# Kernel optimization log

Measured on AMD Instinct MI355X. Metric: run time of the kernel, lower is better.

The kernel has to match this reference:

```python
import jax, jax.numpy as jnp
import numpy as np

B, T, N, D, H, E = 64, 64, 32, 32, 128, 256


def setup_inputs() -> dict:
    key = jax.random.key(0)
    ks = jax.random.split(key, 20)

    def g(k, shape, scale=0.1):
        return (jax.random.normal(k, shape, dtype=jnp.float32) * scale)

    return {
        "ts_batch": jax.random.normal(ks[0], (B, T, N, D), dtype=jnp.float32),
        "edge_index": jax.random.randint(ks[1], (2, E), 0, N, dtype=jnp.int32),
        # encoder: 2-layer GCN-LSTM, gates packed as [i,f,g,o] -> 4H
        "Wen0": g(ks[2], (D + H, 4 * H)), "ben0": jnp.zeros((4 * H,), jnp.float32),
        "Wen1": g(ks[3], (2 * H, 4 * H)), "ben1": jnp.zeros((4 * H,), jnp.float32),
        # decoder: 2-layer GCN-LSTM
        "Wde0": g(ks[4], (D + H, 4 * H)), "bde0": jnp.zeros((4 * H,), jnp.float32),
        "Wde1": g(ks[5], (2 * H, 4 * H)), "bde1": jnp.zeros((4 * H,), jnp.float32),
        # per-node linears (the nn.ModuleList loops, batched as [N, in, out])
        "Wmu": g(ks[6], (N, H, H)), "bmu": jnp.zeros((N, H), jnp.float32),
        "Wlv": g(ks[7], (N, H, H)), "blv": jnp.zeros((N, H), jnp.float32),
        "Who": g(ks[8], (N, H, D)), "bho": jnp.zeros((N, D), jnp.float32),
        "Wholv": g(ks[9], (N, H, D)), "bholv": jnp.zeros((N, D), jnp.float32),
        # reparametrization noise (torch.randn_like), made explicit for determinism
        "eps": jax.random.normal(ks[10], (B, N, H), dtype=jnp.float32),
    }


def reference(ts_batch, edge_index, Wen0, ben0, Wen1, ben1, Wde0, bde0, Wde1, bde1,
              Wmu, bmu, Wlv, blv, Who, bho, Wholv, bholv, eps):
    n = Wmu.shape[0]
    # GCN normalized adjacency with self-loops: D^{-1/2}(A+I)D^{-1/2}
    A = jnp.zeros((n, n), jnp.float32).at[edge_index[1], edge_index[0]].add(1.0)
    A = A + jnp.eye(n, dtype=jnp.float32)
    dinv = jax.lax.rsqrt(A.sum(axis=1))
    A = dinv[:, None] * A * dinv[None, :]

    def gcn(x, W, b):  # x: [B,N,F] -> [B,N,4H]
        return jnp.einsum('ij,bjf->bif', A, x) @ W + b

    def cell(x, h, c, W, b):
        z = gcn(jnp.concatenate([x, h], axis=-1), W, b)
        i, f, g, o = jnp.split(z, 4, axis=-1)
        c = jax.nn.sigmoid(f) * c + jax.nn.sigmoid(i) * jnp.tanh(g)
        h = jax.nn.sigmoid(o) * jnp.tanh(c)
        return h, c

    def pnl(x, W, b):  # per-node linear, replaces the python loop over ModuleList
        return jnp.einsum('bnh,nho->bno', x, W) + b

    bsz, tlen = ts_batch.shape[0], ts_batch.shape[1]
    hdim = Wen0.shape[1] // 4
    z0 = jnp.zeros((bsz, n, hdim), jnp.float32)

    def enc_step(carry, x_t):
        h0, c0, h1, c1 = carry
        h0, c0 = cell(x_t, h0, c0, Wen0, ben0)
        h1, c1 = cell(h0, h1, c1, Wen1, ben1)
        return (h0, c0, h1, c1), None

    (h0, c0, h1, c1), _ = jax.lax.scan(
        enc_step, (z0, z0, z0, z0), jnp.transpose(ts_batch, (1, 0, 2, 3)))

    mu = pnl(h1, Wmu, bmu)
    logvar = pnl(h1, Wlv, blv)
    zlat = mu + eps * jnp.exp(logvar)  # reparametrize (note: exp(logvar), as in source)

    out_last = pnl(zlat, Who, bho)
    outlv_last = pnl(zlat, Wholv, bholv)

    # decoder initialized from encoder final (pre-reparam) hidden state; runs in
    # reverse time feeding back its own output (inference / no teacher forcing)
    def dec_step(carry, _):
        h0, c0, h1, c1, prev = carry
        h0, c0 = cell(prev, h0, c0, Wde0, bde0)
        h1, c1 = cell(h0, h1, c1, Wde1, bde1)
        out = pnl(h1, Who, bho)
        outlv = pnl(h1, Wholv, bholv)
        return (h0, c0, h1, c1, out), (out, outlv)

    _, (outs, outlvs) = jax.lax.scan(
        dec_step, (h0, c0, h1, c1, out_last), None, length=tlen - 1)

    # outs are for timesteps T-2 .. 0; reverse and append step T-1
    output = jnp.concatenate([outs[::-1], out_last[None]], axis=0)
    output_logvar = jnp.concatenate([outlvs[::-1], outlv_last[None]], axis=0)
    output = jnp.transpose(output, (1, 0, 2, 3))            # [B,T,N,D]
    output_logvar = jnp.transpose(output_logvar, (1, 0, 2, 3))
    return output, zlat, mu, logvar, output_logvar
```

## Files before the change

kernel.cpp:

```cpp
#include <hip/hip_runtime.h>


typedef unsigned short u16;
typedef unsigned int u32;
typedef short bf16x8 __attribute__((ext_vector_type(8)));
typedef float f32x4 __attribute__((ext_vector_type(4)));

#define O_OUT 0
#define O_Z   4194304
#define O_MU  4456448
#define O_LV  4718592
#define O_OLV 4980736

#define WS_ABF  0
#define WS_PEN0 1280
#define WS_PEN1 83200
#define WS_PDE0 214272
#define WS_PDE1 296192
#define WS_PHO  427264
#define WS_PLV  558336
#define WS_H1   689408
#define WS_NEED_BYTES 34408960ull

#define XSTR 552

__device__ __forceinline__ u16 f2b(float f){
  unsigned x = __float_as_uint(f);
  x += 0x7fffu + ((x>>16)&1u);
  return (u16)(x>>16);
}
__device__ __forceinline__ float b2f(u16 u){ return __uint_as_float(((unsigned)u)<<16); }
__device__ __forceinline__ float blo(unsigned u){ return __uint_as_float(u<<16); }
__device__ __forceinline__ float bhi(unsigned u){ return __uint_as_float(u & 0xffff0000u); }
__device__ __forceinline__ float sigm(float x){ return 1.f/(1.f+__expf(-x)); }
__device__ __forceinline__ float tanh_(float x){
  float e = __expf(-2.f*fabsf(x));
  float r = (1.f-e)/(1.f+e);
  return __builtin_copysignf(r, x);
}

__global__ void adj_kernel(const int* __restrict__ ei, u16* __restrict__ ws)
{
  __shared__ float As[1024];
  __shared__ float dinv[32];
  const int tid = threadIdx.x;
  for (int e = tid; e < 1024; e += 256) As[e] = 0.f;
  __syncthreads();
  atomicAdd(&As[ei[256 + tid]*32 + ei[tid]], 1.f);
  __syncthreads();
  if (tid < 32) As[tid*33] += 1.f;
  __syncthreads();
  if (tid < 32){
    float s = 0.f;
    for (int j=0;j<32;++j) s += As[tid*32 + j];
    dinv[tid] = rsqrtf(s);
  }
  __syncthreads();
  for (int e = tid; e < 1280; e += 256){
    int i = e / 40, j = e % 40;
    float v = (j < 32) ? As[i*32 + j]*dinv[i]*dinv[j] : 0.f;
    ws[WS_ABF + e] = f2b(v);
  }
}

__global__ void pack_kernel(const float* __restrict__ Wen0, const float* __restrict__ Wen1,
                            const float* __restrict__ Wde0, const float* __restrict__ Wde1,
                            const float* __restrict__ Who,  const float* __restrict__ Wholv,
                            u16* __restrict__ ws)
{
  int id = blockIdx.x*256 + threadIdx.x;
  if (id < 53248){
    const float* W; int KS, dstoff, lid;
    if (id < 10240){ W = Wen0; KS = 5; dstoff = WS_PEN0; lid = id; }
    else if (id < 26624){ W = Wen1; KS = 8; dstoff = WS_PEN1; lid = id - 10240; }
    else if (id < 36864){ W = Wde0; KS = 5; dstoff = WS_PDE0; lid = id - 26624; }
    else { W = Wde1; KS = 8; dstoff = WS_PDE1; lid = id - 36864; }
    int l = lid & 63, rest = lid >> 6;
    int ks = rest % KS, nt = rest / KS;
    int n  = nt*16 + (l & 15);
    int k0 = ks*32 + (l >> 4)*8;
    u16 tmp[8];
    #pragma unroll
    for (int j=0;j<8;++j) tmp[j] = f2b(W[(k0 + j)*512 + n]);
    uint4 v;
    v.x = (unsigned)tmp[0] | ((unsigned)tmp[1] << 16);
    v.y = (unsigned)tmp[2] | ((unsigned)tmp[3] << 16);
    v.z = (unsigned)tmp[4] | ((unsigned)tmp[5] << 16);
    v.w = (unsigned)tmp[6] | ((unsigned)tmp[7] << 16);
    *(uint4*)&ws[dstoff + lid*8] = v;
  } else {
    int e = id - 53248;
    const float* src = (e < 16384) ? Who : Wholv;
    int dsto = (e < 16384) ? WS_PHO : WS_PLV;
    e &= 16383;
    int n = e >> 9, r = e & 511;
    int d = r >> 4, h0 = (r & 15)*8;
    u16 tmp[8];
    #pragma unroll
    for (int j=0;j<8;++j) tmp[j] = f2b(src[(n*128 + h0 + j)*32 + d]);
    uint4 v;
    v.x = (unsigned)tmp[0] | ((unsigned)tmp[1] << 16);
    v.y = (unsigned)tmp[2] | ((unsigned)tmp[3] << 16);
    v.z = (unsigned)tmp[4] | ((unsigned)tmp[5] << 16);
    v.w = (unsigned)tmp[6] | ((unsigned)tmp[7] << 16);
    *(uint4*)&ws[dsto + (n*4096 + d*128 + h0)] = v;
  }
}

template<int KS, int N0>
__device__ __forceinline__ void run_cell(
    const u16* __restrict__ PW, const float* bias4,
    u16* XN, const u16* Abf, u16* yt,
    f32x4 (&cst)[2], int kb0, int kb1, int hwrite,
    int l15, int lq, int wave)
{
  f32x4 acc[2][4];
  #pragma unroll
  for (int mt=0;mt<2;++mt)
    #pragma unroll
    for (int g=0;g<4;++g){ f32x4 z = {0.f,0.f,0.f,0.f}; acc[mt][g] = z; }
  const bf16x8* PW8 = (const bf16x8*)PW;
  const int lane = lq*16 + l15;
  #pragma unroll
  for (int ks=0; ks<KS; ++ks){
    const int off = (ks < N0) ? (kb0 + ks*32) : (kb1 + (ks - N0)*32);
    bf16x8 a0 = *(const bf16x8*)&XN[l15*XSTR + off + lq*8];
    bf16x8 a1 = *(const bf16x8*)&XN[(16 + l15)*XSTR + off + lq*8];
    #pragma unroll
    for (int g=0; g<4; ++g){
      bf16x8 bw = PW8[((g*8 + wave)*KS + ks)*64 + lane];
      acc[0][g] = __builtin_amdgcn_mfma_f32_16x16x32_bf16(a0, bw, acc[0][g], 0, 0, 0);
      acc[1][g] = __builtin_amdgcn_mfma_f32_16x16x32_bf16(a1, bw, acc[1][g], 0, 0, 0);
    }
  }
  f32x4 acc2[2][4];
  u32* yt32 = (u32*)yt;
  bf16x8 afr0 = *(const bf16x8*)&Abf[l15*40 + lq*8];
  bf16x8 afr1 = *(const bf16x8*)&Abf[(16 + l15)*40 + lq*8];
  #pragma unroll
  for (int hh=0; hh<2; ++hh){
    #pragma unroll
    for (int g2=0; g2<2; ++g2){
      const int g = hh*2 + g2;
      #pragma unroll
      for (int mt=0; mt<2; ++mt){
        u32 lo = (u32)f2b(acc[mt][g][0]) | ((u32)f2b(acc[mt][g][1]) << 16);
        u32 hi = (u32)f2b(acc[mt][g][2]) | ((u32)f2b(acc[mt][g][3]) << 16);
        const int base = (g2*16 + l15)*20 + mt*8 + lq*2;
        yt32[base]     = lo;
        yt32[base + 1] = hi;
      }
    }
    #pragma unroll
    for (int g2=0; g2<2; ++g2){
      const int g = hh*2 + g2;
      bf16x8 bfr = *(const bf16x8*)&yt[(g2*16 + l15)*40 + lq*8];
      f32x4 vb = {bias4[g], bias4[g], bias4[g], bias4[g]};
      acc2[0][g] = __builtin_amdgcn_mfma_f32_16x16x32_bf16(afr0, bfr, vb, 0, 0, 0);
      acc2[1][g] = __builtin_amdgcn_mfma_f32_16x16x32_bf16(afr1, bfr, vb, 0, 0, 0);
    }
  }
  const int col = wave*16 + l15;
  #pragma unroll
  for (int mt=0;mt<2;++mt){
    #pragma unroll
    for (int q=0;q<4;++q){
      float iv = sigm(acc2[mt][0][q]);
      float fv = sigm(acc2[mt][1][q]);
      float gv = tanh_(acc2[mt][2][q]);
      float ov = sigm(acc2[mt][3][q]);
      float c  = fv*cst[mt][q] + iv*gv;
      cst[mt][q] = c;
      float h  = ov*tanh_(c);
      XN[(mt*16 + lq*4 + q)*XSTR + hwrite + col] = f2b(h);
    }
  }
}

template<bool SAVE>
__global__ __launch_bounds__(512, 2) void lstm_main(
  const float* __restrict__ ts,
  const float* __restrict__ ben0, const float* __restrict__ ben1,
  const float* __restrict__ bde0, const float* __restrict__ bde1,
  const float* __restrict__ Wmu, const float* __restrict__ bmu,
  const float* __restrict__ Wlv, const float* __restrict__ blv,
  const float* __restrict__ bho, const float* __restrict__ bholv,
  const float* __restrict__ Wholv,
  const float* __restrict__ eps,
  const u16* __restrict__ ws, u16* __restrict__ wsH1,
  float* __restrict__ dout)
{
  __shared__ __align__(16) u16 XN[32*XSTR];
  __shared__ __align__(16) u16 Abf[32*40];
  __shared__ __align__(16) u16 Ytr[8*32*40];
  float* zl = (float*)Ytr;

  const int tid  = threadIdx.x;
  const int lane = tid & 63, wave = tid >> 6;
  const int l15  = lane & 15, lq = lane >> 4;
  const int b    = blockIdx.x;
  u16* yt = Ytr + wave*(32*40);

  for (int e = tid; e < 1280;     e += 512) Abf[e] = ws[WS_ABF + e];
  for (int e = tid; e < 32*XSTR;  e += 512) XN[e] = 0;
  f32x4 c0[2], c1[2];
  {
    f32x4 zz = {0.f,0.f,0.f,0.f};
    c0[0]=c0[1]=c1[0]=c1[1]=zz;
  }
  float biE0[4], biE1[4], biD0[4], biD1[4];
  const int colg = wave*16 + l15;
  #pragma unroll
  for (int g=0; g<4; ++g){
    biE0[g] = ben0[g*128+colg];
    biE1[g] = ben1[g*128+colg];
    biD0[g] = bde0[g*128+colg];
    biD1[g] = bde1[g*128+colg];
  }
  const u16* whoT = ws + WS_PHO;
  const u16* wlvT = ws + WS_PLV;
  __syncthreads();
  {
    const float* xp = ts + (size_t)(b*64)*1024;
    for (int e = tid; e < 1024; e += 512)
      XN[(e >> 5)*XSTR + (e & 31)] = f2b(xp[e]);
  }
  __syncthreads();

  for (int t=0; t<64; ++t){
    const int ph = t & 1;
    run_cell<5,1>(ws+WS_PEN0, biE0, XN, Abf, yt, c0,
                  0, 32 + 128*ph, 32 + 128*(1-ph), l15, lq, wave);
    __syncthreads();
    if (t < 63){
      const float* xp = ts + (size_t)(b*64 + t + 1)*1024;
      for (int e = tid; e < 1024; e += 512)
        XN[(e >> 5)*XSTR + (e & 31)] = f2b(xp[e]);
    }
    run_cell<8,4>(ws+WS_PEN1, biE1, XN, Abf, yt, c1,
                  32 + 128*(1-ph), 288 + 128*ph, 288 + 128*(1-ph), l15, lq, wave);
    __syncthreads();
  }

  for (int k=0;k<8;++k){
    int idx = tid + k*512;
    int n = idx >> 7, o = idx & 127;
    float am = bmu[idx];
    float al = blv[idx];
    for (int h=0; h<128; ++h){
      float hv = b2f(XN[n*XSTR + 288 + h]);
      am += hv * Wmu[(n*128 + h)*128 + o];
      al += hv * Wlv[(n*128 + h)*128 + o];
    }
    float zv = am + eps[b*4096 + idx] * __expf(al);
    zl[idx] = zv;
    dout[O_MU + b*4096 + idx] = am;
    dout[O_LV + b*4096 + idx] = al;
    dout[O_Z  + b*4096 + idx] = zv;
  }
  __syncthreads();
  #pragma unroll
  for (int k=0;k<2;++k){
    int idx = tid + k*512;
    int n = idx >> 5, d = idx & 31;
    float a  = bho[idx];
    float a2 = bholv[idx];
    const u16* wp = whoT + (idx << 7);
    for (int h=0; h<128; ++h){
      float hv = zl[n*128 + h];
      a  += hv * b2f(wp[h]);
      a2 += hv * Wholv[(n*128+h)*32 + d];
    }
    dout[O_OUT + (size_t)(b*64 + 63)*1024 + idx] = a;
    dout[O_OLV + (size_t)(b*64 + 63)*1024 + idx] = a2;
    XN[n*XSTR + d] = f2b(a);
  }
  __syncthreads();

  for (int s=0; s<63; ++s){
    const int pg = s & 1;
    run_cell<5,1>(ws+WS_PDE0, biD0, XN, Abf, yt, c0,
                  0, 32 + 128*pg, 32 + 128*(1-pg), l15, lq, wave);
    __syncthreads();
    run_cell<8,4>(ws+WS_PDE1, biD1, XN, Abf, yt, c1,
                  32 + 128*(1-pg), 288 + 128*pg, 288 + 128*(1-pg), l15, lq, wave);
    __syncthreads();
    const int h1b = 288 + 128*(1-pg);
    if (SAVE){
      u16* dst = wsH1 + (size_t)(b*63 + s)*4096;
      for (int k=0;k<8;++k){
        int idx = tid + k*512;
        dst[idx] = XN[(idx >> 7)*XSTR + h1b + (idx & 127)];
      }
    }
    const int tt = 62 - s;
    #pragma unroll
    for (int k=0;k<2;++k){
      int idx = tid + k*512;
      int n = idx >> 5, d = idx & 31;
      float a = bho[idx];
      const u16* wp = whoT + (idx << 7);
      if (SAVE){
        #pragma unroll 4
        for (int h=0; h<128; h+=8){
          uint4 hv = *(const uint4*)&XN[n*XSTR + h1b + h];
          uint4 wv = *(const uint4*)&wp[h];
          a += blo(hv.x)*blo(wv.x) + bhi(hv.x)*bhi(wv.x);
          a += blo(hv.y)*blo(wv.y) + bhi(hv.y)*bhi(wv.y);
          a += blo(hv.z)*blo(wv.z) + bhi(hv.z)*bhi(wv.z);
          a += blo(hv.w)*blo(wv.w) + bhi(hv.w)*bhi(wv.w);
        }
      } else {
        float a2 = bholv[idx];
        const u16* wp2 = wlvT + (idx << 7);
        #pragma unroll 4
        for (int h=0; h<128; h+=8){
          uint4 hv = *(const uint4*)&XN[n*XSTR + h1b + h];
          uint4 wv = *(const uint4*)&wp[h];
          uint4 w2 = *(const uint4*)&wp2[h];
          float s0=blo(hv.x), s1=bhi(hv.x), s2=blo(hv.y), s3=bhi(hv.y);
          float s4=blo(hv.z), s5=bhi(hv.z), s6=blo(hv.w), s7=bhi(hv.w);
          a  += s0*blo(wv.x) + s1*bhi(wv.x) + s2*blo(wv.y) + s3*bhi(wv.y)
              + s4*blo(wv.z) + s5*bhi(wv.z) + s6*blo(wv.w) + s7*bhi(wv.w);
          a2 += s0*blo(w2.x) + s1*bhi(w2.x) + s2*blo(w2.y) + s3*bhi(w2.y)
              + s4*blo(w2.z) + s5*bhi(w2.z) + s6*blo(w2.w) + s7*bhi(w2.w);
        }
        dout[O_OLV + (size_t)(b*64 + tt)*1024 + idx] = a2;
      }
      dout[O_OUT + (size_t)(b*64 + tt)*1024 + idx] = a;
      XN[n*XSTR + d] = f2b(a);
    }
    __syncthreads();
  }
}

__global__ __launch_bounds__(256) void outlv_kernel(
    const u16* __restrict__ wsH1, const u16* __restrict__ ws,
    const float* __restrict__ bholv, float* __restrict__ dout)
{
  const int n = blockIdx.x, t = blockIdx.y, tid = threadIdx.x;
  __shared__ __align__(16) u16 Ls[64*128];
  const int s = 62 - t;
  for (int e = tid; e < 8192; e += 256){
    int b = e >> 7;
    Ls[e] = wsH1[(size_t)(b*63 + s)*4096 + n*128 + (e & 127)];
  }
  __syncthreads();
  const int d = tid & 31, bq = tid >> 5;
  const u16* wp2 = ws + WS_PLV + ((n*32 + d) << 7);
  const float bias = bholv[n*32 + d];
  for (int b = bq; b < 64; b += 8){
    float acc = bias;
    #pragma unroll 4
    for (int h = 0; h < 128; h += 8){
      uint4 sv = *(const uint4*)&Ls[b*128 + h];
      uint4 wv = *(const uint4*)&wp2[h];
      acc += blo(sv.x)*blo(wv.x) + bhi(sv.x)*bhi(wv.x);
      acc += blo(sv.y)*blo(wv.y) + bhi(sv.y)*bhi(wv.y);
      acc += blo(sv.z)*blo(wv.z) + bhi(sv.z)*bhi(wv.z);
      acc += blo(sv.w)*blo(wv.w) + bhi(sv.w)*bhi(wv.w);
    }
    dout[O_OLV + (size_t)(b*64 + t)*1024 + n*32 + d] = acc;
  }
}

extern "C" void kernel_launch(void* const* d_in, const int* in_sizes, int n_in,
                              void* d_out, int out_size, void* d_ws, size_t ws_size,
                              hipStream_t stream)
{
  (void)in_sizes; (void)n_in; (void)out_size;
  const float* ts   = (const float*)d_in[0];
  const int*   ei   = (const int*)d_in[1];
  const float* Wen0 = (const float*)d_in[2];
  const float* ben0 = (const float*)d_in[3];
  const float* Wen1 = (const float*)d_in[4];
  const float* ben1 = (const float*)d_in[5];
  const float* Wde0 = (const float*)d_in[6];
  const float* bde0 = (const float*)d_in[7];
  const float* Wde1 = (const float*)d_in[8];
  const float* bde1 = (const float*)d_in[9];
  const float* Wmu  = (const float*)d_in[10];
  const float* bmu  = (const float*)d_in[11];
  const float* Wlv  = (const float*)d_in[12];
  const float* blv  = (const float*)d_in[13];
  const float* Who  = (const float*)d_in[14];
  const float* bho  = (const float*)d_in[15];
  const float* Wholv= (const float*)d_in[16];
  const float* bholv= (const float*)d_in[17];
  const float* eps  = (const float*)d_in[18];
  u16*   ws   = (u16*)d_ws;
  float* dout = (float*)d_out;
  const bool save = ws_size >= WS_NEED_BYTES;

  adj_kernel<<<1, 256, 0, stream>>>(ei, ws);
  pack_kernel<<<336, 256, 0, stream>>>(Wen0, Wen1, Wde0, Wde1, Who, Wholv, ws);
  if (save){
    lstm_main<true><<<64, 512, 0, stream>>>(ts, ben0, ben1, bde0, bde1, Wmu, bmu, Wlv, blv,
        bho, bholv, Wholv, eps, ws, ws + WS_H1, dout);
    outlv_kernel<<<dim3(32,63), 256, 0, stream>>>(ws + WS_H1, ws, bholv, dout);
  } else {
    lstm_main<false><<<64, 512, 0, stream>>>(ts, ben0, ben1, bde0, bde1, Wmu, bmu, Wlv, blv,
        bho, bholv, Wholv, eps, ws, ws, dout);
  }
}
```

Before: 2.203 ms.

## Prefetch LSTM weight fragments into registers and split encoder/decoder kernels

Each layer's MFMA weight fragments are now loaded into registers ahead of use, overlapping the global loads with the previous cell's gate math. The fused kernel is split into an encoder kernel and a decoder kernel that hand over hidden and cell state through workspace, which likely frees register pressure per kernel. The Who/Wholv packing layout changes to an hb-major interleave so that neighbouring threads read contiguous 16-byte chunks. The risks are heavy register use from holding 52 bf16x8 fragments, which could cause spills at 2 blocks per CU, plus an extra kernel launch and state round trip.

```diff
diff --git a/kernel.cpp b/kernel.cpp
--- a/kernel.cpp
+++ b/kernel.cpp
@@ -19,8 +19,9 @@
 #define WS_PDE1 296192
 #define WS_PHO  427264
 #define WS_PLV  558336
-#define WS_H1   689408
-#define WS_NEED_BYTES 34408960ull
+#define WS_ST   689408
+#define WS_H1   2786560
+#define WS_NEED_BYTES 38603264ull
 
 #define XSTR 552
 
@@ -94,33 +95,43 @@
     int dsto = (e < 16384) ? WS_PHO : WS_PLV;
     e &= 16383;
     int n = e >> 9, r = e & 511;
-    int d = r >> 4, h0 = (r & 15)*8;
+    int d = r >> 4, hb = r & 15;
     u16 tmp[8];
     #pragma unroll
-    for (int j=0;j<8;++j) tmp[j] = f2b(src[(n*128 + h0 + j)*32 + d]);
+    for (int j=0;j<8;++j) tmp[j] = f2b(src[(n*128 + hb*8 + j)*32 + d]);
     uint4 v;
     v.x = (unsigned)tmp[0] | ((unsigned)tmp[1] << 16);
     v.y = (unsigned)tmp[2] | ((unsigned)tmp[3] << 16);
     v.z = (unsigned)tmp[4] | ((unsigned)tmp[5] << 16);
     v.w = (unsigned)tmp[6] | ((unsigned)tmp[7] << 16);
-    *(uint4*)&ws[dsto + (n*4096 + d*128 + h0)] = v;
-  }
+    *(uint4*)&ws[dsto + (hb*8192 + (n*32 + d)*8)] = v;
+  }
+}
+
+template<int KS>
+__device__ __forceinline__ void prefetch_w(const u16* __restrict__ PW,
+                                           int lane, int wave, bf16x8* dst)
+{
+  const bf16x8* PW8 = (const bf16x8*)PW;
+  #pragma unroll
+  for (int ks=0; ks<KS; ++ks)
+    #pragma unroll
+    for (int g=0; g<4; ++g)
+      dst[ks*4+g] = PW8[((g*8 + wave)*KS + ks)*64 + lane];
 }
 
 template<int KS, int N0>
-__device__ __forceinline__ void run_cell(
-    const u16* __restrict__ PW, const float* bias4,
-    u16* XN, const u16* Abf, u16* yt,
-    f32x4 (&cst)[2], int kb0, int kb1, int hwrite,
-    int l15, int lq, int wave)
+__device__ __forceinline__ void cell_z(
+    const bf16x8* bw, const float* bias4,
+    const u16* XN, const u16* Abf, u16* yt,
+    int kb0, int kb1, int l15, int lq,
+    f32x4 (&acc2)[2][4])
 {
   f32x4 acc[2][4];
   #pragma unroll
   for (int mt=0;mt<2;++mt)
     #pragma unroll
     for (int g=0;g<4;++g){ f32x4 z = {0.f,0.f,0.f,0.f}; acc[mt][g] = z; }
-  const bf16x8* PW8 = (const bf16x8*)PW;
-  const int lane = lq*16 + l15;
   #pragma unroll
   for (int ks=0; ks<KS; ++ks){
     const int off = (ks < N0) ? (kb0 + ks*32) : (kb1 + (ks - N0)*32);
@@ -128,12 +139,10 @@
     bf16x8 a1 = *(const bf16x8*)&XN[(16 + l15)*XSTR + off + lq*8];
     #pragma unroll
     for (int g=0; g<4; ++g){
-      bf16x8 bw = PW8[((g*8 + wave)*KS + ks)*64 + lane];
-      acc[0][g] = __builtin_amdgcn_mfma_f32_16x16x32_bf16(a0, bw, acc[0][g], 0, 0, 0);
-      acc[1][g] = __builtin_amdgcn_mfma_f32_16x16x32_bf16(a1, bw, acc[1][g], 0, 0, 0);
-    }
-  }
-  f32x4 acc2[2][4];
+      acc[0][g] = __builtin_amdgcn_mfma_f32_16x16x32_bf16(a0, bw[ks*4+g], acc[0][g], 0, 0, 0);
+      acc[1][g] = __builtin_amdgcn_mfma_f32_16x16x32_bf16(a1, bw[ks*4+g], acc[1][g], 0, 0, 0);
+    }
+  }
   u32* yt32 = (u32*)yt;
   bf16x8 afr0 = *(const bf16x8*)&Abf[l15*40 + lq*8];
   bf16x8 afr1 = *(const bf16x8*)&Abf[(16 + l15)*40 + lq*8];
@@ -160,7 +169,12 @@
       acc2[1][g] = __builtin_amdgcn_mfma_f32_16x16x32_bf16(afr1, bfr, vb, 0, 0, 0);
     }
   }
-  const int col = wave*16 + l15;
+}
+
+__device__ __forceinline__ void gates(
+    f32x4 (&acc2)[2][4], f32x4 (&cst)[2],
+    u16* XN, int hwrite, int col, int lq)
+{
   #pragma unroll
   for (int mt=0;mt<2;++mt){
     #pragma unroll
@@ -171,23 +185,20 @@
       float ov = sigm(acc2[mt][3][q]);
       float c  = fv*cst[mt][q] + iv*gv;
       cst[mt][q] = c;
-      float h  = ov*tanh_(c);
-      XN[(mt*16 + lq*4 + q)*XSTR + hwrite + col] = f2b(h);
-    }
-  }
-}
-
-template<bool SAVE>
-__global__ __launch_bounds__(512, 2) void lstm_main(
+      XN[(mt*16 + lq*4 + q)*XSTR + hwrite + col] = f2b(ov*tanh_(c));
+    }
+  }
+}
+
+__global__ __launch_bounds__(512, 2) void enc_main(
   const float* __restrict__ ts,
   const float* __restrict__ ben0, const float* __restrict__ ben1,
-  const float* __restrict__ bde0, const float* __restrict__ bde1,
   const float* __restrict__ Wmu, const float* __restrict__ bmu,
   const float* __restrict__ Wlv, const float* __restrict__ blv,
   const float* __restrict__ bho, const float* __restrict__ bholv,
   const float* __restrict__ Wholv,
   const float* __restrict__ eps,
-  const u16* __restrict__ ws, u16* __restrict__ wsH1,
+  const u16* __restrict__ ws, u16* __restrict__ wsST,
   float* __restrict__ dout)
 {
   __shared__ __align__(16) u16 XN[32*XSTR];
@@ -199,26 +210,18 @@
   const int lane = tid & 63, wave = tid >> 6;
   const int l15  = lane & 15, lq = lane >> 4;
   const int b    = blockIdx.x;
+  const int col  = wave*16 + l15;
   u16* yt = Ytr + wave*(32*40);
 
-  for (int e = tid; e < 1280;     e += 512) Abf[e] = ws[WS_ABF + e];
-  for (int e = tid; e < 32*XSTR;  e += 512) XN[e] = 0;
+  for (int e = tid; e < 1280;    e += 512) Abf[e] = ws[WS_ABF + e];
+  for (int e = tid; e < 32*XSTR; e += 512) XN[e] = 0;
   f32x4 c0[2], c1[2];
-  {
-    f32x4 zz = {0.f,0.f,0.f,0.f};
-    c0[0]=c0[1]=c1[0]=c1[1]=zz;
-  }
-  float biE0[4], biE1[4], biD0[4], biD1[4];
-  const int colg = wave*16 + l15;
-  #pragma unroll
-  for (int g=0; g<4; ++g){
-    biE0[g] = ben0[g*128+colg];
-    biE1[g] = ben1[g*128+colg];
-    biD0[g] = bde0[g*128+colg];
-    biD1[g] = bde1[g*128+colg];
-  }
-  const u16* whoT = ws + WS_PHO;
-  const u16* wlvT = ws + WS_PLV;
+  { f32x4 zz = {0.f,0.f,0.f,0.f}; c0[0]=c0[1]=c1[0]=c1[1]=zz; }
+  float biE0[4], biE1[4];
+  #pragma unroll
+  for (int g=0; g<4; ++g){ biE0[g] = ben0[g*128+col]; biE1[g] = ben1[g*128+col]; }
+  bf16x8 w0[20], w1[32];
+  prefetch_w<5>(ws+WS_PEN0, lane, wave, w0);
   __syncthreads();
   {
     const float* xp = ts + (size_t)(b*64)*1024;
@@ -229,16 +232,19 @@
 
   for (int t=0; t<64; ++t){
     const int ph = t & 1;
-    run_cell<5,1>(ws+WS_PEN0, biE0, XN, Abf, yt, c0,
-                  0, 32 + 128*ph, 32 + 128*(1-ph), l15, lq, wave);
+    f32x4 z0[2][4], z1[2][4];
+    cell_z<5,1>(w0, biE0, XN, Abf, yt, 0, 32 + 128*ph, l15, lq, z0);
+    prefetch_w<8>(ws+WS_PEN1, lane, wave, w1);
+    gates(z0, c0, XN, 32 + 128*(1-ph), col, lq);
     __syncthreads();
     if (t < 63){
       const float* xp = ts + (size_t)(b*64 + t + 1)*1024;
       for (int e = tid; e < 1024; e += 512)
         XN[(e >> 5)*XSTR + (e & 31)] = f2b(xp[e]);
     }
-    run_cell<8,4>(ws+WS_PEN1, biE1, XN, Abf, yt, c1,
-                  32 + 128*(1-ph), 288 + 128*ph, 288 + 128*(1-ph), l15, lq, wave);
+    cell_z<8,4>(w1, biE1, XN, Abf, yt, 32 + 128*(1-ph), 288 + 128*ph, l15, lq, z1);
+    if (t < 63) prefetch_w<5>(ws+WS_PEN0, lane, wave, w0);
+    gates(z1, c1, XN, 288 + 128*(1-ph), col, lq);
     __syncthreads();
   }
 
@@ -247,6 +253,7 @@
     int n = idx >> 7, o = idx & 127;
     float am = bmu[idx];
     float al = blv[idx];
+    #pragma unroll 4
     for (int h=0; h<128; ++h){
       float hv = b2f(XN[n*XSTR + 288 + h]);
       am += hv * Wmu[(n*128 + h)*128 + o];
@@ -259,31 +266,104 @@
     dout[O_Z  + b*4096 + idx] = zv;
   }
   __syncthreads();
+  const u16* whoP = ws + WS_PHO;
   #pragma unroll
   for (int k=0;k<2;++k){
     int idx = tid + k*512;
     int n = idx >> 5, d = idx & 31;
     float a  = bho[idx];
     float a2 = bholv[idx];
-    const u16* wp = whoT + (idx << 7);
-    for (int h=0; h<128; ++h){
-      float hv = zl[n*128 + h];
-      a  += hv * b2f(wp[h]);
-      a2 += hv * Wholv[(n*128+h)*32 + d];
-    }
+    #pragma unroll 4
+    for (int hb=0; hb<16; ++hb){
+      uint4 wv = *(const uint4*)&whoP[hb*8192 + idx*8];
+      const float* zp = &zl[n*128 + hb*8];
+      a += zp[0]*blo(wv.x) + zp[1]*bhi(wv.x) + zp[2]*blo(wv.y) + zp[3]*bhi(wv.y)
+         + zp[4]*blo(wv.z) + zp[5]*bhi(wv.z) + zp[6]*blo(wv.w) + zp[7]*bhi(wv.w);
+    }
+    for (int h=0; h<128; ++h)
+      a2 += zl[n*128 + h] * Wholv[(n*128+h)*32 + d];
     dout[O_OUT + (size_t)(b*64 + 63)*1024 + idx] = a;
     dout[O_OLV + (size_t)(b*64 + 63)*1024 + idx] = a2;
     XN[n*XSTR + d] = f2b(a);
   }
   __syncthreads();
+  u16* st = wsST + (size_t)b*32768;
+  for (int e = tid; e < 4096; e += 512){
+    st[e]        = XN[(e >> 7)*XSTR + 32  + (e & 127)];
+    st[4096 + e] = XN[(e >> 7)*XSTR + 288 + (e & 127)];
+  }
+  for (int e = tid; e < 1024; e += 512)
+    st[8192 + e] = XN[(e >> 5)*XSTR + (e & 31)];
+  float* cs0 = (float*)(st + 10240);
+  float* cs1 = (float*)(st + 18432);
+  #pragma unroll
+  for (int mt=0;mt<2;++mt)
+    #pragma unroll
+    for (int q=0;q<4;++q){
+      int node = mt*16 + lq*4 + q;
+      cs0[node*128 + col] = c0[mt][q];
+      cs1[node*128 + col] = c1[mt][q];
+    }
+}
+
+template<bool SAVE>
+__global__ __launch_bounds__(512, 2) void dec_main(
+  const float* __restrict__ bde0, const float* __restrict__ bde1,
+  const float* __restrict__ bho, const float* __restrict__ bholv,
+  const u16* __restrict__ ws, const u16* __restrict__ wsST, u16* __restrict__ wsH1,
+  float* __restrict__ dout)
+{
+  __shared__ __align__(16) u16 XN[32*XSTR];
+  __shared__ __align__(16) u16 Abf[32*40];
+  __shared__ __align__(16) u16 Ytr[8*32*40];
+
+  const int tid  = threadIdx.x;
+  const int lane = tid & 63, wave = tid >> 6;
+  const int l15  = lane & 15, lq = lane >> 4;
+  const int b    = blockIdx.x;
+  const int col  = wave*16 + l15;
+  u16* yt = Ytr + wave*(32*40);
+
+  for (int e = tid; e < 1280; e += 512) Abf[e] = ws[WS_ABF + e];
+  const u16* st = wsST + (size_t)b*32768;
+  for (int e = tid; e < 4096; e += 512){
+    XN[(e >> 7)*XSTR + 32  + (e & 127)] = st[e];
+    XN[(e >> 7)*XSTR + 288 + (e & 127)] = st[4096 + e];
+  }
+  for (int e = tid; e < 1024; e += 512)
+    XN[(e >> 5)*XSTR + (e & 31)] = st[8192 + e];
+  f32x4 c0[2], c1[2];
+  {
+    const float* cs0 = (const float*)(st + 10240);
+    const float* cs1 = (const float*)(st + 18432);
+    #pragma unroll
+    for (int mt=0;mt<2;++mt)
+      #pragma unroll
+      for (int q=0;q<4;++q){
+        int node = mt*16 + lq*4 + q;
+        c0[mt][q] = cs0[node*128 + col];
+        c1[mt][q] = cs1[node*128 + col];
+      }
+  }
+  float biD0[4], biD1[4];
+  #pragma unroll
+  for (int g=0; g<4; ++g){ biD0[g] = bde0[g*128+col]; biD1[g] = bde1[g*128+col]; }
+  const u16* whoP = ws + WS_PHO;
+  const u16* wlvP = ws + WS_PLV;
+  bf16x8 w0[20], w1[32];
+  prefetch_w<5>(ws+WS_PDE0, lane, wave, w0);
+  __syncthreads();
 
   for (int s=0; s<63; ++s){
     const int pg = s & 1;
-    run_cell<5,1>(ws+WS_PDE0, biD0, XN, Abf, yt, c0,
-                  0, 32 + 128*pg, 32 + 128*(1-pg), l15, lq, wave);
+    f32x4 z0[2][4], z1[2][4];
+    cell_z<5,1>(w0, biD0, XN, Abf, yt, 0, 32 + 128*pg, l15, lq, z0);
+    prefetch_w<8>(ws+WS_PDE1, lane, wave, w1);
+    gates(z0, c0, XN, 32 + 128*(1-pg), col, lq);
     __syncthreads();
-    run_cell<8,4>(ws+WS_PDE1, biD1, XN, Abf, yt, c1,
-                  32 + 128*(1-pg), 288 + 128*pg, 288 + 128*(1-pg), l15, lq, wave);
+    cell_z<8,4>(w1, biD1, XN, Abf, yt, 32 + 128*(1-pg), 288 + 128*pg, l15, lq, z1);
+    if (s < 62) prefetch_w<5>(ws+WS_PDE0, lane, wave, w0);
+    gates(z1, c1, XN, 288 + 128*(1-pg), col, lq);
     __syncthreads();
     const int h1b = 288 + 128*(1-pg);
     if (SAVE){
@@ -299,12 +379,11 @@
       int idx = tid + k*512;
       int n = idx >> 5, d = idx & 31;
       float a = bho[idx];
-      const u16* wp = whoT + (idx << 7);
       if (SAVE){
         #pragma unroll 4
-        for (int h=0; h<128; h+=8){
-          uint4 hv = *(const uint4*)&XN[n*XSTR + h1b + h];
-          uint4 wv = *(const uint4*)&wp[h];
+        for (int hb=0; hb<16; ++hb){
+          uint4 hv = *(const uint4*)&XN[n*XSTR + h1b + hb*8];
+          uint4 wv = *(const uint4*)&whoP[hb*8192 + idx*8];
           a += blo(hv.x)*blo(wv.x) + bhi(hv.x)*bhi(wv.x);
           a += blo(hv.y)*blo(wv.y) + bhi(hv.y)*bhi(wv.y);
           a += blo(hv.z)*blo(wv.z) + bhi(hv.z)*bhi(wv.z);
@@ -312,12 +391,11 @@
         }
       } else {
         float a2 = bholv[idx];
-        const u16* wp2 = wlvT + (idx << 7);
         #pragma unroll 4
-        for (int h=0; h<128; h+=8){
-          uint4 hv = *(const uint4*)&XN[n*XSTR + h1b + h];
-          uint4 wv = *(const uint4*)&wp[h];
-          uint4 w2 = *(const uint4*)&wp2[h];
+        for (int hb=0; hb<16; ++hb){
+          uint4 hv = *(const uint4*)&XN[n*XSTR + h1b + hb*8];
+          uint4 wv = *(const uint4*)&whoP[hb*8192 + idx*8];
+          uint4 w2 = *(const uint4*)&wlvP[hb*8192 + idx*8];
           float s0=blo(hv.x), s1=bhi(hv.x), s2=blo(hv.y), s3=bhi(hv.y);
           float s4=blo(hv.z), s5=bhi(hv.z), s6=blo(hv.w), s7=bhi(hv.w);
           a  += s0*blo(wv.x) + s1*bhi(wv.x) + s2*blo(wv.y) + s3*bhi(wv.y)
@@ -347,14 +425,13 @@
   }
   __syncthreads();
   const int d = tid & 31, bq = tid >> 5;
-  const u16* wp2 = ws + WS_PLV + ((n*32 + d) << 7);
   const float bias = bholv[n*32 + d];
   for (int b = bq; b < 64; b += 8){
     float acc = bias;
     #pragma unroll 4
-    for (int h = 0; h < 128; h += 8){
-      uint4 sv = *(const uint4*)&Ls[b*128 + h];
-      uint4 wv = *(const uint4*)&wp2[h];
+    for (int hb = 0; hb < 16; ++hb){
+      uint4 sv = *(const uint4*)&Ls[b*128 + hb*8];
+      uint4 wv = *(const uint4*)&ws[WS_PLV + hb*8192 + (n*32 + d)*8];
       acc += blo(sv.x)*blo(wv.x) + bhi(sv.x)*bhi(wv.x);
       acc += blo(sv.y)*blo(wv.y) + bhi(sv.y)*bhi(wv.y);
       acc += blo(sv.z)*blo(wv.z) + bhi(sv.z)*bhi(wv.z);
@@ -394,12 +471,14 @@
 
   adj_kernel<<<1, 256, 0, stream>>>(ei, ws);
   pack_kernel<<<336, 256, 0, stream>>>(Wen0, Wen1, Wde0, Wde1, Who, Wholv, ws);
+  enc_main<<<64, 512, 0, stream>>>(ts, ben0, ben1, Wmu, bmu, Wlv, blv,
+      bho, bholv, Wholv, eps, ws, ws + WS_ST, dout);
   if (save){
-    lstm_main<true><<<64, 512, 0, stream>>>(ts, ben0, ben1, bde0, bde1, Wmu, bmu, Wlv, blv,
-        bho, bholv, Wholv, eps, ws, ws + WS_H1, dout);
+    dec_main<true><<<64, 512, 0, stream>>>(bde0, bde1, bho, bholv,
+        ws, ws + WS_ST, ws + WS_H1, dout);
     outlv_kernel<<<dim3(32,63), 256, 0, stream>>>(ws + WS_H1, ws, bholv, dout);
   } else {
-    lstm_main<false><<<64, 512, 0, stream>>>(ts, ben0, ben1, bde0, bde1, Wmu, bmu, Wlv, blv,
-        bho, bholv, Wholv, eps, ws, ws, dout);
-  }
-}
+    dec_main<false><<<64, 512, 0, stream>>>(bde0, bde1, bho, bholv,
+        ws, ws + WS_ST, ws, dout);
+  }
+}
```

New measurement: 2.547 ms. 15.6% more time.

## Double block to 1024 threads splitting row tiles across waves, drop h ping-pong

Applied to the files above, without the earlier changes.

Each batch block now runs 16 waves instead of 8, with each wave handling one 16-row tile and one gate column group, which halves per-wave MFMA and activation work on the serial recurrence. The per-wave transpose scratch becomes a shared Yt buffer, so an extra barrier is needed inside each cell. The double-buffered hidden-state columns are removed, shrinking XN, and the Who/Wholv packed layout is rearranged to interleave by 8-element h chunks so that 1024 threads each compute one output with coalesced loads. The cost is more barriers per step and higher register pressure under the new launch bounds.

```diff
diff --git a/kernel.cpp b/kernel.cpp
--- a/kernel.cpp
+++ b/kernel.cpp
@@ -22,7 +22,7 @@
 #define WS_H1   689408
 #define WS_NEED_BYTES 34408960ull
 
-#define XSTR 552
+#define XSTR 296
 
 __device__ __forceinline__ u16 f2b(float f){
   unsigned x = __float_as_uint(f);
@@ -94,91 +94,74 @@
     int dsto = (e < 16384) ? WS_PHO : WS_PLV;
     e &= 16383;
     int n = e >> 9, r = e & 511;
-    int d = r >> 4, h0 = (r & 15)*8;
+    int d = r >> 4, hb = r & 15;
     u16 tmp[8];
     #pragma unroll
-    for (int j=0;j<8;++j) tmp[j] = f2b(src[(n*128 + h0 + j)*32 + d]);
+    for (int j=0;j<8;++j) tmp[j] = f2b(src[(n*128 + hb*8 + j)*32 + d]);
     uint4 v;
     v.x = (unsigned)tmp[0] | ((unsigned)tmp[1] << 16);
     v.y = (unsigned)tmp[2] | ((unsigned)tmp[3] << 16);
     v.z = (unsigned)tmp[4] | ((unsigned)tmp[5] << 16);
     v.w = (unsigned)tmp[6] | ((unsigned)tmp[7] << 16);
-    *(uint4*)&ws[dsto + (n*4096 + d*128 + h0)] = v;
+    *(uint4*)&ws[dsto + (hb*8192 + (n*32 + d)*8)] = v;
   }
 }
 
 template<int KS, int N0>
 __device__ __forceinline__ void run_cell(
     const u16* __restrict__ PW, const float* bias4,
-    u16* XN, const u16* Abf, u16* yt,
-    f32x4 (&cst)[2], int kb0, int kb1, int hwrite,
-    int l15, int lq, int wave)
-{
-  f32x4 acc[2][4];
-  #pragma unroll
-  for (int mt=0;mt<2;++mt)
-    #pragma unroll
-    for (int g=0;g<4;++g){ f32x4 z = {0.f,0.f,0.f,0.f}; acc[mt][g] = z; }
+    u16* XN, const u16* Abf, u16* Yt,
+    f32x4 &cst, int kb0, int kb1, int hw,
+    int cg, int mt, int l15, int lq)
+{
+  f32x4 acc[4];
+  #pragma unroll
+  for (int g=0;g<4;++g){ f32x4 z = {0.f,0.f,0.f,0.f}; acc[g] = z; }
   const bf16x8* PW8 = (const bf16x8*)PW;
   const int lane = lq*16 + l15;
   #pragma unroll
   for (int ks=0; ks<KS; ++ks){
     const int off = (ks < N0) ? (kb0 + ks*32) : (kb1 + (ks - N0)*32);
-    bf16x8 a0 = *(const bf16x8*)&XN[l15*XSTR + off + lq*8];
-    bf16x8 a1 = *(const bf16x8*)&XN[(16 + l15)*XSTR + off + lq*8];
+    bf16x8 a = *(const bf16x8*)&XN[(mt*16 + l15)*XSTR + off + lq*8];
     #pragma unroll
     for (int g=0; g<4; ++g){
-      bf16x8 bw = PW8[((g*8 + wave)*KS + ks)*64 + lane];
-      acc[0][g] = __builtin_amdgcn_mfma_f32_16x16x32_bf16(a0, bw, acc[0][g], 0, 0, 0);
-      acc[1][g] = __builtin_amdgcn_mfma_f32_16x16x32_bf16(a1, bw, acc[1][g], 0, 0, 0);
-    }
-  }
-  f32x4 acc2[2][4];
-  u32* yt32 = (u32*)yt;
-  bf16x8 afr0 = *(const bf16x8*)&Abf[l15*40 + lq*8];
-  bf16x8 afr1 = *(const bf16x8*)&Abf[(16 + l15)*40 + lq*8];
-  #pragma unroll
-  for (int hh=0; hh<2; ++hh){
-    #pragma unroll
-    for (int g2=0; g2<2; ++g2){
-      const int g = hh*2 + g2;
-      #pragma unroll
-      for (int mt=0; mt<2; ++mt){
-        u32 lo = (u32)f2b(acc[mt][g][0]) | ((u32)f2b(acc[mt][g][1]) << 16);
-        u32 hi = (u32)f2b(acc[mt][g][2]) | ((u32)f2b(acc[mt][g][3]) << 16);
-        const int base = (g2*16 + l15)*20 + mt*8 + lq*2;
-        yt32[base]     = lo;
-        yt32[base + 1] = hi;
-      }
-    }
-    #pragma unroll
-    for (int g2=0; g2<2; ++g2){
-      const int g = hh*2 + g2;
-      bf16x8 bfr = *(const bf16x8*)&yt[(g2*16 + l15)*40 + lq*8];
-      f32x4 vb = {bias4[g], bias4[g], bias4[g], bias4[g]};
-      acc2[0][g] = __builtin_amdgcn_mfma_f32_16x16x32_bf16(afr0, bfr, vb, 0, 0, 0);
-      acc2[1][g] = __builtin_amdgcn_mfma_f32_16x16x32_bf16(afr1, bfr, vb, 0, 0, 0);
-    }
-  }
-  const int col = wave*16 + l15;
-  #pragma unroll
-  for (int mt=0;mt<2;++mt){
-    #pragma unroll
-    for (int q=0;q<4;++q){
-      float iv = sigm(acc2[mt][0][q]);
-      float fv = sigm(acc2[mt][1][q]);
-      float gv = tanh_(acc2[mt][2][q]);
-      float ov = sigm(acc2[mt][3][q]);
-      float c  = fv*cst[mt][q] + iv*gv;
-      cst[mt][q] = c;
-      float h  = ov*tanh_(c);
-      XN[(mt*16 + lq*4 + q)*XSTR + hwrite + col] = f2b(h);
-    }
+      bf16x8 bw = PW8[((g*8 + cg)*KS + ks)*64 + lane];
+      acc[g] = __builtin_amdgcn_mfma_f32_16x16x32_bf16(a, bw, acc[g], 0, 0, 0);
+    }
+  }
+  u32* yt32 = (u32*)Yt;
+  #pragma unroll
+  for (int g=0; g<4; ++g){
+    u32 lo = (u32)f2b(acc[g][0]) | ((u32)f2b(acc[g][1]) << 16);
+    u32 hi = (u32)f2b(acc[g][2]) | ((u32)f2b(acc[g][3]) << 16);
+    const int base = (g*8 + cg)*320 + l15*20 + mt*8 + lq*2;
+    yt32[base]     = lo;
+    yt32[base + 1] = hi;
+  }
+  __syncthreads();
+  bf16x8 afr = *(const bf16x8*)&Abf[(mt*16 + l15)*40 + lq*8];
+  f32x4 acc2[4];
+  #pragma unroll
+  for (int g=0; g<4; ++g){
+    bf16x8 bfr = *(const bf16x8*)&Yt[(g*8 + cg)*640 + l15*40 + lq*8];
+    f32x4 vb = {bias4[g], bias4[g], bias4[g], bias4[g]};
+    acc2[g] = __builtin_amdgcn_mfma_f32_16x16x32_bf16(afr, bfr, vb, 0, 0, 0);
+  }
+  const int col = cg*16 + l15;
+  #pragma unroll
+  for (int q=0;q<4;++q){
+    float iv = sigm(acc2[0][q]);
+    float fv = sigm(acc2[1][q]);
+    float gv = tanh_(acc2[2][q]);
+    float ov = sigm(acc2[3][q]);
+    float c  = fv*cst[q] + iv*gv;
+    cst[q] = c;
+    XN[(mt*16 + lq*4 + q)*XSTR + hw + col] = f2b(ov*tanh_(c));
   }
 }
 
 template<bool SAVE>
-__global__ __launch_bounds__(512, 2) void lstm_main(
+__global__ __launch_bounds__(1024, 4) void lstm_main(
   const float* __restrict__ ts,
   const float* __restrict__ ben0, const float* __restrict__ ben1,
   const float* __restrict__ bde0, const float* __restrict__ bde1,
@@ -192,63 +175,56 @@
 {
   __shared__ __align__(16) u16 XN[32*XSTR];
   __shared__ __align__(16) u16 Abf[32*40];
-  __shared__ __align__(16) u16 Ytr[8*32*40];
-  float* zl = (float*)Ytr;
+  __shared__ __align__(16) u16 Yt[32*640];
+  float* zl = (float*)Yt;
 
   const int tid  = threadIdx.x;
   const int lane = tid & 63, wave = tid >> 6;
   const int l15  = lane & 15, lq = lane >> 4;
+  const int cg   = wave & 7,  mt = wave >> 3;
+  const int col  = cg*16 + l15;
   const int b    = blockIdx.x;
-  u16* yt = Ytr + wave*(32*40);
-
-  for (int e = tid; e < 1280;     e += 512) Abf[e] = ws[WS_ABF + e];
-  for (int e = tid; e < 32*XSTR;  e += 512) XN[e] = 0;
-  f32x4 c0[2], c1[2];
-  {
-    f32x4 zz = {0.f,0.f,0.f,0.f};
-    c0[0]=c0[1]=c1[0]=c1[1]=zz;
-  }
+
+  for (int e = tid; e < 1280;    e += 1024) Abf[e] = ws[WS_ABF + e];
+  for (int e = tid; e < 32*XSTR; e += 1024) XN[e] = 0;
+  f32x4 c0, c1;
+  { f32x4 zz = {0.f,0.f,0.f,0.f}; c0 = zz; c1 = zz; }
   float biE0[4], biE1[4], biD0[4], biD1[4];
-  const int colg = wave*16 + l15;
   #pragma unroll
   for (int g=0; g<4; ++g){
-    biE0[g] = ben0[g*128+colg];
-    biE1[g] = ben1[g*128+colg];
-    biD0[g] = bde0[g*128+colg];
-    biD1[g] = bde1[g*128+colg];
-  }
-  const u16* whoT = ws + WS_PHO;
-  const u16* wlvT = ws + WS_PLV;
+    biE0[g] = ben0[g*128+col];
+    biE1[g] = ben1[g*128+col];
+    biD0[g] = bde0[g*128+col];
+    biD1[g] = bde1[g*128+col];
+  }
+  const u16* whoP = ws + WS_PHO;
+  const u16* wlvP = ws + WS_PLV;
   __syncthreads();
   {
     const float* xp = ts + (size_t)(b*64)*1024;
-    for (int e = tid; e < 1024; e += 512)
-      XN[(e >> 5)*XSTR + (e & 31)] = f2b(xp[e]);
+    XN[(tid >> 5)*XSTR + (tid & 31)] = f2b(xp[tid]);
   }
   __syncthreads();
 
   for (int t=0; t<64; ++t){
-    const int ph = t & 1;
-    run_cell<5,1>(ws+WS_PEN0, biE0, XN, Abf, yt, c0,
-                  0, 32 + 128*ph, 32 + 128*(1-ph), l15, lq, wave);
+    run_cell<5,1>(ws+WS_PEN0, biE0, XN, Abf, Yt, c0, 0, 32, 32, cg, mt, l15, lq);
     __syncthreads();
     if (t < 63){
       const float* xp = ts + (size_t)(b*64 + t + 1)*1024;
-      for (int e = tid; e < 1024; e += 512)
-        XN[(e >> 5)*XSTR + (e & 31)] = f2b(xp[e]);
-    }
-    run_cell<8,4>(ws+WS_PEN1, biE1, XN, Abf, yt, c1,
-                  32 + 128*(1-ph), 288 + 128*ph, 288 + 128*(1-ph), l15, lq, wave);
-    __syncthreads();
-  }
-
-  for (int k=0;k<8;++k){
-    int idx = tid + k*512;
+      XN[(tid >> 5)*XSTR + (tid & 31)] = f2b(xp[tid]);
+    }
+    run_cell<8,4>(ws+WS_PEN1, biE1, XN, Abf, Yt, c1, 32, 160, 160, cg, mt, l15, lq);
+    __syncthreads();
+  }
+
+  for (int k=0;k<4;++k){
+    int idx = tid + k*1024;
     int n = idx >> 7, o = idx & 127;
     float am = bmu[idx];
     float al = blv[idx];
+    #pragma unroll 4
     for (int h=0; h<128; ++h){
-      float hv = b2f(XN[n*XSTR + 288 + h]);
+      float hv = b2f(XN[n*XSTR + 160 + h]);
       am += hv * Wmu[(n*128 + h)*128 + o];
       al += hv * Wlv[(n*128 + h)*128 + o];
     }
@@ -259,65 +235,67 @@
     dout[O_Z  + b*4096 + idx] = zv;
   }
   __syncthreads();
-  #pragma unroll
-  for (int k=0;k<2;++k){
-    int idx = tid + k*512;
-    int n = idx >> 5, d = idx & 31;
-    float a  = bho[idx];
-    float a2 = bholv[idx];
-    const u16* wp = whoT + (idx << 7);
-    for (int h=0; h<128; ++h){
-      float hv = zl[n*128 + h];
-      a  += hv * b2f(wp[h]);
-      a2 += hv * Wholv[(n*128+h)*32 + d];
-    }
-    dout[O_OUT + (size_t)(b*64 + 63)*1024 + idx] = a;
-    dout[O_OLV + (size_t)(b*64 + 63)*1024 + idx] = a2;
+  {
+    int n = tid >> 5, d = tid & 31;
+    float a  = bho[tid];
+    float a2 = bholv[tid];
+    #pragma unroll 4
+    for (int hb=0; hb<16; ++hb){
+      uint4 wv = *(const uint4*)&whoP[hb*8192 + tid*8];
+      const float* zp = &zl[n*128 + hb*8];
+      a += zp[0]*blo(wv.x) + zp[1]*bhi(wv.x) + zp[2]*blo(wv.y) + zp[3]*bhi(wv.y)
+         + zp[4]*blo(wv.z) + zp[5]*bhi(wv.z) + zp[6]*blo(wv.w) + zp[7]*bhi(wv.w);
+    }
+    for (int h=0; h<128; ++h)
+      a2 += zl[n*128 + h] * Wholv[(n*128+h)*32 + d];
+    dout[O_OUT + (size_t)(b*64 + 63)*1024 + tid] = a;
+    dout[O_OLV + (size_t)(b*64 + 63)*1024 + tid] = a2;
+    __syncthreads();
     XN[n*XSTR + d] = f2b(a);
   }
   __syncthreads();
 
   for (int s=0; s<63; ++s){
-    const int pg = s & 1;
-    run_cell<5,1>(ws+WS_PDE0, biD0, XN, Abf, yt, c0,
-                  0, 32 + 128*pg, 32 + 128*(1-pg), l15, lq, wave);
-    __syncthreads();
-    run_cell<8,4>(ws+WS_PDE1, biD1, XN, Abf, yt, c1,
-                  32 + 128*(1-pg), 288 + 128*pg, 288 + 128*(1-pg), l15, lq, wave);
-    __syncthreads();
-    const int h1b = 288 + 128*(1-pg);
+    run_cell<5,1>(ws+WS_PDE0, biD0, XN, Abf, Yt, c0, 0, 32, 32, cg, mt, l15, lq);
+    __syncthreads();
+    run_cell<8,4>(ws+WS_PDE1, biD1, XN, Abf, Yt, c1, 32, 160, 160, cg, mt, l15, lq);
+    __syncthreads();
     if (SAVE){
       u16* dst = wsH1 + (size_t)(b*63 + s)*4096;
-      for (int k=0;k<8;++k){
-        int idx = tid + k*512;
-        dst[idx] = XN[(idx >> 7)*XSTR + h1b + (idx & 127)];
+      #pragma unroll
+      for (int k=0;k<4;++k){
+        int idx = tid + k*1024;
+        dst[idx] = XN[(idx >> 7)*XSTR + 160 + (idx & 127)];
       }
     }
     const int tt = 62 - s;
-    #pragma unroll
-    for (int k=0;k<2;++k){
-      int idx = tid + k*512;
-      int n = idx >> 5, d = idx & 31;
-      float a = bho[idx];
-      const u16* wp = whoT + (idx << 7);
+    {
+      int n = tid >> 5, d = tid & 31;
+      float a = bho[tid], ab = 0.f;
       if (SAVE){
         #pragma unroll 4
-        for (int h=0; h<128; h+=8){
-          uint4 hv = *(const uint4*)&XN[n*XSTR + h1b + h];
-          uint4 wv = *(const uint4*)&wp[h];
-          a += blo(hv.x)*blo(wv.x) + bhi(hv.x)*bhi(wv.x);
-          a += blo(hv.y)*blo(wv.y) + bhi(hv.y)*bhi(wv.y);
-          a += blo(hv.z)*blo(wv.z) + bhi(hv.z)*bhi(wv.z);
-          a += blo(hv.w)*blo(wv.w) + bhi(hv.w)*bhi(wv.w);
+        for (int hb=0; hb<16; hb+=2){
+          uint4 hv = *(const uint4*)&XN[n*XSTR + 160 + hb*8];
+          uint4 wv = *(const uint4*)&whoP[hb*8192 + tid*8];
+          uint4 h2 = *(const uint4*)&XN[n*XSTR + 160 + hb*8 + 8];
+          uint4 w2 = *(const uint4*)&whoP[(hb+1)*8192 + tid*8];
+          a  += blo(hv.x)*blo(wv.x) + bhi(hv.x)*bhi(wv.x)
+              + blo(hv.y)*blo(wv.y) + bhi(hv.y)*bhi(wv.y)
+              + blo(hv.z)*blo(wv.z) + bhi(hv.z)*bhi(wv.z)
+              + blo(hv.w)*blo(wv.w) + bhi(hv.w)*bhi(wv.w);
+          ab += blo(h2.x)*blo(w2.x) + bhi(h2.x)*bhi(w2.x)
+              + blo(h2.y)*blo(w2.y) + bhi(h2.y)*bhi(w2.y)
+              + blo(h2.z)*blo(w2.z) + bhi(h2.z)*bhi(w2.z)
+              + blo(h2.w)*blo(w2.w) + bhi(h2.w)*bhi(w2.w);
         }
+        a += ab;
       } else {
-        float a2 = bholv[idx];
-        const u16* wp2 = wlvT + (idx << 7);
+        float a2 = bholv[tid];
         #pragma unroll 4
-        for (int h=0; h<128; h+=8){
-          uint4 hv = *(const uint4*)&XN[n*XSTR + h1b + h];
-          uint4 wv = *(const uint4*)&wp[h];
-          uint4 w2 = *(const uint4*)&wp2[h];
+        for (int hb=0; hb<16; ++hb){
+          uint4 hv = *(const uint4*)&XN[n*XSTR + 160 + hb*8];
+          uint4 wv = *(const uint4*)&whoP[hb*8192 + tid*8];
+          uint4 w2 = *(const uint4*)&wlvP[hb*8192 + tid*8];
           float s0=blo(hv.x), s1=bhi(hv.x), s2=blo(hv.y), s3=bhi(hv.y);
           float s4=blo(hv.z), s5=bhi(hv.z), s6=blo(hv.w), s7=bhi(hv.w);
           a  += s0*blo(wv.x) + s1*bhi(wv.x) + s2*blo(wv.y) + s3*bhi(wv.y)
@@ -325,9 +303,9 @@
           a2 += s0*blo(w2.x) + s1*bhi(w2.x) + s2*blo(w2.y) + s3*bhi(w2.y)
               + s4*blo(w2.z) + s5*bhi(w2.z) + s6*blo(w2.w) + s7*bhi(w2.w);
         }
-        dout[O_OLV + (size_t)(b*64 + tt)*1024 + idx] = a2;
+        dout[O_OLV + (size_t)(b*64 + tt)*1024 + tid] = a2;
       }
-      dout[O_OUT + (size_t)(b*64 + tt)*1024 + idx] = a;
+      dout[O_OUT + (size_t)(b*64 + tt)*1024 + tid] = a;
       XN[n*XSTR + d] = f2b(a);
     }
     __syncthreads();
@@ -347,14 +325,13 @@
   }
   __syncthreads();
   const int d = tid & 31, bq = tid >> 5;
-  const u16* wp2 = ws + WS_PLV + ((n*32 + d) << 7);
   const float bias = bholv[n*32 + d];
   for (int b = bq; b < 64; b += 8){
     float acc = bias;
     #pragma unroll 4
-    for (int h = 0; h < 128; h += 8){
-      uint4 sv = *(const uint4*)&Ls[b*128 + h];
-      uint4 wv = *(const uint4*)&wp2[h];
+    for (int hb = 0; hb < 16; ++hb){
+      uint4 sv = *(const uint4*)&Ls[b*128 + hb*8];
+      uint4 wv = *(const uint4*)&ws[WS_PLV + hb*8192 + (n*32 + d)*8];
       acc += blo(sv.x)*blo(wv.x) + bhi(sv.x)*bhi(wv.x);
       acc += blo(sv.y)*blo(wv.y) + bhi(sv.y)*bhi(wv.y);
       acc += blo(sv.z)*blo(wv.z) + bhi(sv.z)*bhi(wv.z);
@@ -395,11 +372,11 @@
   adj_kernel<<<1, 256, 0, stream>>>(ei, ws);
   pack_kernel<<<336, 256, 0, stream>>>(Wen0, Wen1, Wde0, Wde1, Who, Wholv, ws);
   if (save){
-    lstm_main<true><<<64, 512, 0, stream>>>(ts, ben0, ben1, bde0, bde1, Wmu, bmu, Wlv, blv,
+    lstm_main<true><<<64, 1024, 0, stream>>>(ts, ben0, ben1, bde0, bde1, Wmu, bmu, Wlv, blv,
         bho, bholv, Wholv, eps, ws, ws + WS_H1, dout);
     outlv_kernel<<<dim3(32,63), 256, 0, stream>>>(ws + WS_H1, ws, bholv, dout);
   } else {
-    lstm_main<false><<<64, 512, 0, stream>>>(ts, ben0, ben1, bde0, bde1, Wmu, bmu, Wlv, blv,
+    lstm_main<false><<<64, 1024, 0, stream>>>(ts, ben0, ben1, bde0, bde1, Wmu, bmu, Wlv, blv,
         bho, bholv, Wholv, eps, ws, ws, dout);
   }
 }
```

New measurement: 3.752 ms. 70.3% more time.
